# Performance work log

Hardware: AMD Instinct MI355X
Metric: run time of the kernel (lower is better)

Reference implementation:

```python
import jax, jax.numpy as jnp
import numpy as np

B, T, N, F = 16, 12, 1000, 64
K_CHEB, OUT = 3, 64


def setup_inputs() -> dict:
    key = jax.random.key(0)
    k1, k2, k3, k4 = jax.random.split(key, 4)
    x = jax.random.normal(k1, (B, T, N, F), dtype=jnp.float32)
    SAtt = jax.random.uniform(k2, (B, N, N), dtype=jnp.float32)
    cheb = jax.random.normal(k3, (K_CHEB, N, N), dtype=jnp.float32) * 0.05
    Theta = jax.random.normal(k4, (K_CHEB, F, OUT), dtype=jnp.float32) * 0.05
    return {"x": x, "SAtt": SAtt, "cheb": cheb, "Theta": Theta}


def reference(x, SAtt, cheb, Theta):
    # Attention-masked Chebyshev polynomials: A[b,k,i,j] = cheb[k,i,j] * SAtt[b,i,j]
    A = cheb[None, :, :, :] * SAtt[:, None, :, :]          # (B,K,N,N)
    # rhs[b,t,k,i,f] = sum_j A[b,k,j,i] * x[b,t,j,f]  (transpose of A in original code)
    rhs = jnp.einsum('bkji,btjf->btkif', A, x)             # (B,T,K,N,F)
    # accumulate over k with per-k feature transform Theta[k]
    out = jnp.einsum('btkif,kfo->btio', rhs, Theta)        # (B,T,N,OUT)
    return jax.nn.relu(out)
```

## Files before the change

### kernel.cpp

```cpp
#include <hip/hip_runtime.h>

#define B_  16
#define T_  12
#define N_  1000
#define F_  64
#define KC  3
#define O_  64
#define NP  1024
#define KP  (KC * NP)
#define CC  (T_ * O_)

typedef __bf16 bf16x8 __attribute__((ext_vector_type(8)));
typedef float  f32x4  __attribute__((ext_vector_type(4)));
typedef float  f32x16 __attribute__((ext_vector_type(16)));

__device__ __forceinline__ unsigned short f2bf(float f) {
  __bf16 h = (__bf16)f;
  return __builtin_bit_cast(unsigned short, h);
}

__device__ __forceinline__ void gl_lds16(const void* g, void* l) {
  __builtin_amdgcn_global_load_lds(
      (const __attribute__((address_space(1))) unsigned int*)g,
      (__attribute__((address_space(3))) unsigned int*)l,
      16, 0, 0);
}

__global__ __launch_bounds__(256) void k_prep(
    const float* __restrict__ x, const float* __restrict__ SAtt,
    const float* __restrict__ cheb, const float* __restrict__ Theta,
    unsigned short* __restrict__ ASt, unsigned short* __restrict__ Yt) {
  __shared__ union {
    struct { unsigned short prod[KC][64][66]; } s1;
    struct {
      unsigned short thl[KC][64][72];
      unsigned short xl[64][72];
      unsigned short ot[64][72];
    } s2;
  } sm;
  const int tid = threadIdx.x;
  const int bid = blockIdx.x;

  if (bid < 4096) {
    const int ib = (bid & 15) * 64, jb = ((bid >> 4) & 15) * 64, b = bid >> 8;
    const int ii4 = (tid & 15) * 4, jr = tid >> 4;
#pragma unroll
    for (int p = 0; p < 4; ++p) {
      const int jj = p * 16 + jr;
      const int gj = jb + jj;
      const int gjc = gj < N_ ? gj : N_ - 1;
      const int gi = ib + ii4;
      const bool iok = gi < N_;
      const bool ok = iok && (gj < N_);
      float4 s4 = make_float4(0.f, 0.f, 0.f, 0.f);
      if (iok) s4 = *(const float4*)&SAtt[((size_t)b * N_ + gjc) * N_ + gi];
#pragma unroll
      for (int k = 0; k < KC; ++k) {
        float4 c4 = make_float4(0.f, 0.f, 0.f, 0.f);
        if (iok) c4 = *(const float4*)&cheb[((size_t)k * N_ + gjc) * N_ + gi];
        ushort2 lo, hi;
        lo.x = ok ? f2bf(c4.x * s4.x) : (unsigned short)0;
        lo.y = ok ? f2bf(c4.y * s4.y) : (unsigned short)0;
        hi.x = ok ? f2bf(c4.z * s4.z) : (unsigned short)0;
        hi.y = ok ? f2bf(c4.w * s4.w) : (unsigned short)0;
        *(ushort2*)&sm.s1.prod[k][jj][ii4]     = lo;
        *(ushort2*)&sm.s1.prod[k][jj][ii4 + 2] = hi;
      }
    }
    __syncthreads();
    const int j8 = (tid & 7) * 8, i0 = tid >> 3;
#pragma unroll
    for (int p = 0; p < 2; ++p) {
      const int iw = p * 32 + i0;
#pragma unroll
      for (int k = 0; k < KC; ++k) {
        unsigned short v[8];
#pragma unroll
        for (int m = 0; m < 8; ++m) v[m] = sm.s1.prod[k][j8 + m][iw];
        *(uint4*)&ASt[((size_t)(b * NP + ib + iw) * KC + k) * NP + jb + j8] =
            *(uint4*)v;
      }
    }
  } else {
    const int b2 = bid - 4096;
    const int jb = (b2 & 15) * 64, bt = b2 >> 4;
#pragma unroll
    for (int it = 0; it < 12; ++it) {
      const int e = (tid + it * 256) * 4;
      const int k = e >> 12, f = (e >> 6) & 63, o0 = e & 63;
      const float4 v = *(const float4*)&Theta[e];
      sm.s2.thl[k][o0 + 0][f] = f2bf(v.x);
      sm.s2.thl[k][o0 + 1][f] = f2bf(v.y);
      sm.s2.thl[k][o0 + 2][f] = f2bf(v.z);
      sm.s2.thl[k][o0 + 3][f] = f2bf(v.w);
    }
    const float* xrow = x + ((size_t)bt * N_ + jb) * F_;
#pragma unroll
    for (int p = 0; p < 4; ++p) {
      const int i4 = tid + p * 256;
      const int fl = i4 * 4, j = fl >> 6, f = fl & 63;
      float4 v;
      if (jb + j < N_) v = ((const float4*)xrow)[i4];
      else             v = make_float4(0.f, 0.f, 0.f, 0.f);
      ushort4 u;
      u.x = f2bf(v.x); u.y = f2bf(v.y); u.z = f2bf(v.z); u.w = f2bf(v.w);
      *(ushort4*)&sm.s2.xl[j][f] = u;
    }
    __syncthreads();

    const int w = tid >> 6, l = tid & 63, quad = l >> 4, lr = l & 15;
    const int os = tid >> 2, q = tid & 3;
#pragma unroll
    for (int k = 0; k < KC; ++k) {
      f32x4 acc[4];
#pragma unroll
      for (int mi = 0; mi < 4; ++mi) acc[mi] = (f32x4){0.f, 0.f, 0.f, 0.f};
#pragma unroll
      for (int ks = 0; ks < 2; ++ks) {
        const int fo = ks * 32 + quad * 8;
        const bf16x8 bb = *(const bf16x8*)&sm.s2.xl[w * 16 + lr][fo];
#pragma unroll
        for (int mi = 0; mi < 4; ++mi) {
          const bf16x8 a = *(const bf16x8*)&sm.s2.thl[k][mi * 16 + lr][fo];
          acc[mi] =
              __builtin_amdgcn_mfma_f32_16x16x32_bf16(a, bb, acc[mi], 0, 0, 0);
        }
      }
      __syncthreads();
#pragma unroll
      for (int mi = 0; mi < 4; ++mi)
#pragma unroll
        for (int r = 0; r < 4; ++r)
          sm.s2.ot[mi * 16 + quad * 4 + r][w * 16 + lr] = f2bf(acc[mi][r]);
      __syncthreads();
      unsigned short* yrow = &Yt[((size_t)(bt * O_ + os) * KC + k) * NP + jb];
      *(uint4*)&yrow[q * 8]      = *(const uint4*)&sm.s2.ot[os][q * 8];
      *(uint4*)&yrow[32 + q * 8] = *(const uint4*)&sm.s2.ot[os][32 + q * 8];
    }
  }
}

__global__ __launch_bounds__(256, 2) void k_gemm(
    const unsigned short* __restrict__ ASt, const unsigned short* __restrict__ Yt,
    float* __restrict__ out) {
  __shared__ unsigned short Al[128 * 64];
  __shared__ unsigned short Bl[128 * 64];
  const int tid = threadIdx.x;
  const int bid = blockIdx.x;
  const int xcd = bid & 7, s = bid >> 3;
  const int b = xcd * 2 + (s / 48);
  const int r48 = s % 48;
  const int ib = (r48 / 6) * 128, cb = (r48 % 6) * 128;

  const unsigned short* Abase = ASt + ((size_t)b * NP + ib) * KP;
  const unsigned short* Bbase = Yt + ((size_t)b * CC + cb) * KP;
  const int w = tid >> 6, l = tid & 63;
  const int l32 = l & 31, lh = l >> 5;
  const int wr = w & 1, wc = w >> 1;
  const int lrow = l >> 3, lchunk = l & 7;
  const int src_chunk = lchunk ^ lrow;

  f32x16 acc[2][2];
#pragma unroll
  for (int mi = 0; mi < 2; ++mi)
#pragma unroll
    for (int ci = 0; ci < 2; ++ci)
      acc[mi][ci] = (f32x16){0.f};

  const int swz = l32 & 7;

  for (int kt = 0; kt < KP / 64; ++kt) {
    __syncthreads();
    const int k0 = kt * 64;
#pragma unroll
    for (int s4 = 0; s4 < 4; ++s4) {
      const int row = w * 32 + s4 * 8;
      gl_lds16(Abase + (size_t)(row + lrow) * KP + k0 + src_chunk * 8,
               &Al[row * 64]);
    }
#pragma unroll
    for (int s4 = 0; s4 < 4; ++s4) {
      const int row = w * 32 + s4 * 8;
      gl_lds16(Bbase + (size_t)(row + lrow) * KP + k0 + src_chunk * 8,
               &Bl[row * 64]);
    }
    __syncthreads();
#pragma unroll
    for (int ks = 0; ks < 4; ++ks) {
      const int chunk = ks * 2 + lh;
      const int pc = (chunk ^ swz) * 8;
      bf16x8 a[2], bb[2];
#pragma unroll
      for (int mi = 0; mi < 2; ++mi)
        a[mi] = *(const bf16x8*)&Al[(wr * 64 + mi * 32 + l32) * 64 + pc];
#pragma unroll
      for (int ci = 0; ci < 2; ++ci)
        bb[ci] = *(const bf16x8*)&Bl[(wc * 64 + ci * 32 + l32) * 64 + pc];
#pragma unroll
      for (int mi = 0; mi < 2; ++mi)
#pragma unroll
        for (int ci = 0; ci < 2; ++ci)
          acc[mi][ci] = __builtin_amdgcn_mfma_f32_32x32x16_bf16(
              a[mi], bb[ci], acc[mi][ci], 0, 0, 0);
    }
  }

#pragma unroll
  for (int mi = 0; mi < 2; ++mi) {
#pragma unroll
    for (int ci = 0; ci < 2; ++ci) {
      const int c = cb + wc * 64 + ci * 32 + l32;
      const int t = c >> 6, o = c & 63;
      float* orow = out + ((size_t)(b * T_ + t) * N_) * O_ + o;
#pragma unroll
      for (int r = 0; r < 16; ++r) {
        const int i = ib + wr * 64 + mi * 32 + (r & 3) + 8 * (r >> 2) + 4 * lh;
        if (i < N_) {
          const float v = acc[mi][ci][r];
          orow[(size_t)i * O_] = v > 0.f ? v : 0.f;
        }
      }
    }
  }
}

extern "C" void kernel_launch(void* const* d_in, const int* in_sizes, int n_in,
                              void* d_out, int out_size, void* d_ws, size_t ws_size,
                              hipStream_t stream) {
  const float* x     = (const float*)d_in[0];
  const float* SAtt  = (const float*)d_in[1];
  const float* cheb  = (const float*)d_in[2];
  const float* Theta = (const float*)d_in[3];
  float* out = (float*)d_out;

  unsigned short* ASt = (unsigned short*)d_ws;
  unsigned short* Yt  = ASt + (size_t)B_ * NP * KC * NP;

  k_prep<<<4096 + 3072, 256, 0, stream>>>(x, SAtt, cheb, Theta, ASt, Yt);
  k_gemm<<<768, 256, 0, stream>>>(ASt, Yt, out);
}
```

Baseline: 326.6 us.

## Pre-swizzle GEMM operands into MFMA fragment order and load directly from global

The prep kernel now writes the masked Chebyshev matrix and the Theta-transformed features in a per-wave, per-MFMA-fragment packed layout. The GEMM then drops shared memory and barriers, with each lane loading its bf16x8 fragments straight from global memory in fully coalesced 1KB segments, and occupancy is raised to 3 blocks per CU. This removes LDS staging and synchronisation cost. In exchange, operand tiles are no longer shared across waves through LDS, so each A/B fragment is read by two waves from global/L2, and there is no explicit prefetching to hide latency.

```diff
diff --git a/kernel.cpp b/kernel.cpp
--- a/kernel.cpp
+++ b/kernel.cpp
@@ -9,6 +9,7 @@
 #define NP  1024
 #define KP  (KC * NP)
 #define CC  (T_ * O_)
+#define NKT 48
 
 typedef __bf16 bf16x8 __attribute__((ext_vector_type(8)));
 typedef float  f32x4  __attribute__((ext_vector_type(4)));
@@ -19,17 +20,11 @@
   return __builtin_bit_cast(unsigned short, h);
 }
 
-__device__ __forceinline__ void gl_lds16(const void* g, void* l) {
-  __builtin_amdgcn_global_load_lds(
-      (const __attribute__((address_space(1))) unsigned int*)g,
-      (__attribute__((address_space(3))) unsigned int*)l,
-      16, 0, 0);
-}
 
 __global__ __launch_bounds__(256) void k_prep(
     const float* __restrict__ x, const float* __restrict__ SAtt,
     const float* __restrict__ cheb, const float* __restrict__ Theta,
-    unsigned short* __restrict__ ASt, unsigned short* __restrict__ Yt) {
+    unsigned short* __restrict__ AF, unsigned short* __restrict__ BF) {
   __shared__ union {
     struct { unsigned short prod[KC][64][66]; } s1;
     struct {
@@ -40,9 +35,13 @@
   } sm;
   const int tid = threadIdx.x;
   const int bid = blockIdx.x;
+  const int l = tid & 63, ksw = tid >> 6;
+  const int i32 = l & 31, lh = l >> 5;
 
   if (bid < 4096) {
-    const int ib = (bid & 15) * 64, jb = ((bid >> 4) & 15) * 64, b = bid >> 8;
+    const int ib64 = bid & 15, jb64 = (bid >> 4) & 15, b = bid >> 8;
+    const int ib = ib64 * 64, jb = jb64 * 64;
+    const int ibt = ib64 >> 1, wr = ib64 & 1;
     const int ii4 = (tid & 15) * 4, jr = tid >> 4;
 #pragma unroll
     for (int p = 0; p < 4; ++p) {
@@ -68,22 +67,26 @@
       }
     }
     __syncthreads();
-    const int j8 = (tid & 7) * 8, i0 = tid >> 3;
 #pragma unroll
     for (int p = 0; p < 2; ++p) {
-      const int iw = p * 32 + i0;
+      const int iw = p * 32 + i32;
 #pragma unroll
       for (int k = 0; k < KC; ++k) {
+        const int kt = k * 16 + jb64;
         unsigned short v[8];
 #pragma unroll
-        for (int m = 0; m < 8; ++m) v[m] = sm.s1.prod[k][j8 + m][iw];
-        *(uint4*)&ASt[((size_t)(b * NP + ib + iw) * KC + k) * NP + jb + j8] =
-            *(uint4*)v;
+        for (int e = 0; e < 8; ++e)
+          v[e] = sm.s1.prod[k][(ksw * 2 + lh) * 8 + e][iw];
+        const size_t seg =
+            ((((((size_t)b * 8 + ibt) * 2 + wr) * 2 + p) * NKT + kt) * 4 + ksw);
+        *(uint4*)&AF[seg * 512 + l * 8] = *(uint4*)v;
       }
     }
   } else {
     const int b2 = bid - 4096;
     const int jb = (b2 & 15) * 64, bt = b2 >> 4;
+    const int b = bt / T_, t = bt % T_;
+    const int cbt = t >> 1, wcs = t & 1;
 #pragma unroll
     for (int it = 0; it < 12; ++it) {
       const int e = (tid + it * 256) * 4;
@@ -108,8 +111,7 @@
     }
     __syncthreads();
 
-    const int w = tid >> 6, l = tid & 63, quad = l >> 4, lr = l & 15;
-    const int os = tid >> 2, q = tid & 3;
+    const int w = tid >> 6, quad = l >> 4, lr = l & 15;
 #pragma unroll
     for (int k = 0; k < KC; ++k) {
       f32x4 acc[4];
@@ -133,32 +135,46 @@
         for (int r = 0; r < 4; ++r)
           sm.s2.ot[mi * 16 + quad * 4 + r][w * 16 + lr] = f2bf(acc[mi][r]);
       __syncthreads();
-      unsigned short* yrow = &Yt[((size_t)(bt * O_ + os) * KC + k) * NP + jb];
-      *(uint4*)&yrow[q * 8]      = *(const uint4*)&sm.s2.ot[os][q * 8];
-      *(uint4*)&yrow[32 + q * 8] = *(const uint4*)&sm.s2.ot[os][32 + q * 8];
+      const int kt = k * 16 + (jb >> 6);
+#pragma unroll
+      for (int ci = 0; ci < 2; ++ci) {
+        const int o = ci * 32 + i32;
+        unsigned short v[8];
+#pragma unroll
+        for (int e = 0; e < 8; ++e)
+          v[e] = sm.s2.ot[o][ksw * 16 + lh * 8 + e];
+        const size_t seg =
+            ((((((size_t)b * 6 + cbt) * 2 + wcs) * 2 + ci) * NKT + kt) * 4 + ksw);
+        *(uint4*)&BF[seg * 512 + l * 8] = *(uint4*)v;
+      }
     }
   }
 }
 
-__global__ __launch_bounds__(256, 2) void k_gemm(
-    const unsigned short* __restrict__ ASt, const unsigned short* __restrict__ Yt,
+__global__ __launch_bounds__(256, 3) void k_gemm(
+    const unsigned short* __restrict__ AF, const unsigned short* __restrict__ BF,
     float* __restrict__ out) {
-  __shared__ unsigned short Al[128 * 64];
-  __shared__ unsigned short Bl[128 * 64];
   const int tid = threadIdx.x;
   const int bid = blockIdx.x;
   const int xcd = bid & 7, s = bid >> 3;
   const int b = xcd * 2 + (s / 48);
   const int r48 = s % 48;
-  const int ib = (r48 / 6) * 128, cb = (r48 % 6) * 128;
-
-  const unsigned short* Abase = ASt + ((size_t)b * NP + ib) * KP;
-  const unsigned short* Bbase = Yt + ((size_t)b * CC + cb) * KP;
+  const int ibt = r48 / 6, cbt = r48 % 6;
+
   const int w = tid >> 6, l = tid & 63;
+  const int wr = w & 1, wc = w >> 1;
   const int l32 = l & 31, lh = l >> 5;
-  const int wr = w & 1, wc = w >> 1;
-  const int lrow = l >> 3, lchunk = l & 7;
-  const int src_chunk = lchunk ^ lrow;
+
+  const unsigned short* Aw[2];
+  const unsigned short* Bw[2];
+#pragma unroll
+  for (int mi = 0; mi < 2; ++mi)
+    Aw[mi] = AF +
+        ((((size_t)b * 8 + ibt) * 2 + wr) * 2 + mi) * (NKT * 4 * 512) + l * 8;
+#pragma unroll
+  for (int ci = 0; ci < 2; ++ci)
+    Bw[ci] = BF +
+        ((((size_t)b * 6 + cbt) * 2 + wc) * 2 + ci) * (NKT * 4 * 512) + l * 8;
 
   f32x16 acc[2][2];
 #pragma unroll
@@ -167,44 +183,22 @@
     for (int ci = 0; ci < 2; ++ci)
       acc[mi][ci] = (f32x16){0.f};
 
-  const int swz = l32 & 7;
-
-  for (int kt = 0; kt < KP / 64; ++kt) {
-    __syncthreads();
-    const int k0 = kt * 64;
-#pragma unroll
-    for (int s4 = 0; s4 < 4; ++s4) {
-      const int row = w * 32 + s4 * 8;
-      gl_lds16(Abase + (size_t)(row + lrow) * KP + k0 + src_chunk * 8,
-               &Al[row * 64]);
-    }
-#pragma unroll
-    for (int s4 = 0; s4 < 4; ++s4) {
-      const int row = w * 32 + s4 * 8;
-      gl_lds16(Bbase + (size_t)(row + lrow) * KP + k0 + src_chunk * 8,
-               &Bl[row * 64]);
-    }
-    __syncthreads();
+  for (int kt = 0; kt < NKT; ++kt) {
 #pragma unroll
     for (int ks = 0; ks < 4; ++ks) {
-      const int chunk = ks * 2 + lh;
-      const int pc = (chunk ^ swz) * 8;
-      bf16x8 a[2], bb[2];
-#pragma unroll
-      for (int mi = 0; mi < 2; ++mi)
-        a[mi] = *(const bf16x8*)&Al[(wr * 64 + mi * 32 + l32) * 64 + pc];
-#pragma unroll
-      for (int ci = 0; ci < 2; ++ci)
-        bb[ci] = *(const bf16x8*)&Bl[(wc * 64 + ci * 32 + l32) * 64 + pc];
-#pragma unroll
-      for (int mi = 0; mi < 2; ++mi)
-#pragma unroll
-        for (int ci = 0; ci < 2; ++ci)
-          acc[mi][ci] = __builtin_amdgcn_mfma_f32_32x32x16_bf16(
-              a[mi], bb[ci], acc[mi][ci], 0, 0, 0);
+      const size_t off = ((size_t)kt * 4 + ks) * 512;
+      const bf16x8 a0 = *(const bf16x8*)(Aw[0] + off);
+      const bf16x8 a1 = *(const bf16x8*)(Aw[1] + off);
+      const bf16x8 b0 = *(const bf16x8*)(Bw[0] + off);
+      const bf16x8 b1 = *(const bf16x8*)(Bw[1] + off);
+      acc[0][0] = __builtin_amdgcn_mfma_f32_32x32x16_bf16(a0, b0, acc[0][0], 0, 0, 0);
+      acc[0][1] = __builtin_amdgcn_mfma_f32_32x32x16_bf16(a0, b1, acc[0][1], 0, 0, 0);
+      acc[1][0] = __builtin_amdgcn_mfma_f32_32x32x16_bf16(a1, b0, acc[1][0], 0, 0, 0);
+      acc[1][1] = __builtin_amdgcn_mfma_f32_32x32x16_bf16(a1, b1, acc[1][1], 0, 0, 0);
     }
   }
 
+  const int ib = ibt * 128, cb = cbt * 128;
 #pragma unroll
   for (int mi = 0; mi < 2; ++mi) {
 #pragma unroll
@@ -233,9 +227,9 @@
   const float* Theta = (const float*)d_in[3];
   float* out = (float*)d_out;
 
-  unsigned short* ASt = (unsigned short*)d_ws;
-  unsigned short* Yt  = ASt + (size_t)B_ * NP * KC * NP;
-
-  k_prep<<<4096 + 3072, 256, 0, stream>>>(x, SAtt, cheb, Theta, ASt, Yt);
-  k_gemm<<<768, 256, 0, stream>>>(ASt, Yt, out);
-}
+  unsigned short* AF = (unsigned short*)d_ws;
+  unsigned short* BF = AF + (size_t)B_ * NP * KC * NP;
+
+  k_prep<<<4096 + 3072, 256, 0, stream>>>(x, SAtt, cheb, Theta, AF, BF);
+  k_gemm<<<768, 256, 0, stream>>>(AF, BF, out);
+}
```

After: 361.9 us. +10.8%, slower.
